# Optimization experiments

Measured on AMD Instinct MI355X. Metric: run time of the kernel, lower is better.

Reference implementation:

```python
import jax, jax.numpy as jnp
import numpy as np

B, L = 128, 100
VOCAB, WORD_D = 50000, 100
TAG_NUM, TAG_D = 52, 20
POS_NUM, POS_D = 202, 20
HID = 256                 # hidden_size = NUM_CAPS * CAP_D
NUM_CAPS, CAP_D = 16, 16
N_CLASS = 19
ROUTING_ITER = 3
IN_D = WORD_D + TAG_D + 2 * POS_D  # 160
ENTITY_MARK = 68          # pos value marking the entity token


def setup_inputs() -> dict:
    key = jax.random.key(0)
    ks = jax.random.split(key, 20)
    s = 0.05
    word = jax.random.randint(ks[0], (B, L), 0, VOCAB)
    tag = jax.random.randint(ks[1], (B, L), 0, TAG_NUM)
    pos1 = jax.random.randint(ks[2], (B, L), 0, POS_NUM)
    pos2 = jax.random.randint(ks[3], (B, L), 0, POS_NUM)
    # guarantee exactly one ENTITY_MARK per row (getEntityFeature's .index(68))
    pos1 = jnp.where(pos1 == ENTITY_MARK, ENTITY_MARK + 1, pos1)
    pos2 = jnp.where(pos2 == ENTITY_MARK, ENTITY_MARK + 1, pos2)
    e1 = jax.random.randint(ks[4], (B,), 0, L)
    e2 = jax.random.randint(ks[5], (B,), 0, L)
    pos1 = pos1.at[jnp.arange(B), e1].set(ENTITY_MARK)
    pos2 = pos2.at[jnp.arange(B), e2].set(ENTITY_MARK)
    # embedding tables (padding_idx 0 rows zeroed for tag/pos, as in torch)
    word_emb = jax.random.normal(ks[6], (VOCAB, WORD_D), jnp.float32) * s
    tag_emb = (jax.random.normal(ks[7], (TAG_NUM, TAG_D), jnp.float32) * s).at[0].set(0.0)
    pos1_emb = (jax.random.normal(ks[8], (POS_NUM, POS_D), jnp.float32) * s).at[0].set(0.0)
    pos2_emb = (jax.random.normal(ks[9], (POS_NUM, POS_D), jnp.float32) * s).at[0].set(0.0)
    # BiLSTM params (torch gate order i,f,g,o stacked along first axis)
    def lstm_params(k):
        k1, k2 = jax.random.split(k)
        w_ih = jax.random.normal(k1, (4 * HID, IN_D), jnp.float32) * s
        w_hh = jax.random.normal(k2, (4 * HID, HID), jnp.float32) * s
        return w_ih, w_hh, jnp.zeros((4 * HID,), jnp.float32), jnp.zeros((4 * HID,), jnp.float32)
    w_ih_f, w_hh_f, b_ih_f, b_hh_f = lstm_params(ks[10])
    w_ih_b, w_hh_b, b_ih_b, b_hh_b = lstm_params(ks[11])
    # digit-caps transform [in_caps, in_dim, out_caps*out_dim]
    W_caps = jax.random.normal(ks[12], (NUM_CAPS * L, CAP_D, N_CLASS * CAP_D), jnp.float32) * s
    b_route = jnp.zeros((NUM_CAPS * L, N_CLASS), jnp.float32)  # routing logit prior (learned)
    return {"word": word, "tag": tag, "pos1": pos1, "pos2": pos2,
            "word_emb": word_emb, "tag_emb": tag_emb, "pos1_emb": pos1_emb, "pos2_emb": pos2_emb,
            "w_ih_f": w_ih_f, "w_hh_f": w_hh_f, "b_ih_f": b_ih_f, "b_hh_f": b_hh_f,
            "w_ih_b": w_ih_b, "w_hh_b": w_hh_b, "b_ih_b": b_ih_b, "b_hh_b": b_hh_b,
            "W_caps": W_caps, "b_route": b_route}


def _lstm_dir(x, w_ih, w_hh, b_ih, b_hh, reverse):
    # x: [B, L, IN_D] -> h: [B, L, HID]
    xg = jnp.einsum('bld,gd->blg', x, w_ih) + b_ih + b_hh  # precompute input gates
    def step(carry, g):
        h, c = carry
        g = g + h @ w_hh.T
        i, f, gg, o = jnp.split(g, 4, axis=-1)
        c = jax.nn.sigmoid(f) * c + jax.nn.sigmoid(i) * jnp.tanh(gg)
        h = jax.nn.sigmoid(o) * jnp.tanh(c)
        return (h, c), h
    init = (jnp.zeros((x.shape[0], HID), x.dtype), jnp.zeros((x.shape[0], HID), x.dtype))
    _, hs = jax.lax.scan(step, init, jnp.swapaxes(xg, 0, 1), reverse=reverse)
    return jnp.swapaxes(hs, 0, 1)


def _squash(x, axis=-1):
    n2 = jnp.sum(x * x, axis=axis, keepdims=True)
    return x * (n2 / (1.0 + n2)) / jnp.sqrt(n2 + 1e-9)


def reference(word, tag, pos1, pos2, word_emb, tag_emb, pos1_emb, pos2_emb,
              w_ih_f, w_hh_f, b_ih_f, b_hh_f, w_ih_b, w_hh_b, b_ih_b, b_hh_b,
              W_caps, b_route):
    # embed + concat (dropout = identity in eval mode)
    emb = jnp.concatenate([word_emb[word], tag_emb[tag], pos1_emb[pos1], pos2_emb[pos2]], axis=-1)
    hf = _lstm_dir(emb, w_ih_f, w_hh_f, b_ih_f, b_hh_f, reverse=False)
    hb = _lstm_dir(emb, w_ih_b, w_hh_b, b_ih_b, b_hh_b, reverse=True)
    x = hf + hb  # sum of direction halves == x[:,:,:H] + x[:,:,H:2H]
    # vectorized entity gather: first index where pos == 68
    bidx = jnp.arange(x.shape[0])
    e1 = jnp.argmax(pos1 == ENTITY_MARK, axis=1)
    e2 = jnp.argmax(pos2 == ENTITY_MARK, axis=1)
    he = x[bidx, e1] + x[bidx, e2]  # [B, HID]
    # primary capsules: [B, L*NUM_CAPS, CAP_D], squashed per capsule
    u = _squash(x.reshape(x.shape[0], L * NUM_CAPS, CAP_D))
    # entity-guided attention over words, broadcast to capsules
    att = jax.nn.softmax(jnp.einsum('bld,bd->bl', x, he), axis=1)  # [B, L]
    alpha = jnp.repeat(att, NUM_CAPS, axis=1)  # [B, L*NUM_CAPS]
    # digit caps predictions: [B, in_caps, N_CLASS, CAP_D]
    u_hat = jnp.einsum('bic,ico->bio', u, W_caps).reshape(x.shape[0], L * NUM_CAPS, N_CLASS, CAP_D)
    # attention-weighted agreement routing
    bb = jnp.broadcast_to(b_route, (x.shape[0],) + b_route.shape)
    v = None
    for _ in range(ROUTING_ITER):
        c = jax.nn.softmax(bb, axis=-1) * alpha[:, :, None]  # coupling * attention
        s = jnp.einsum('bio,biod->bod', c, u_hat)
        v = _squash(s)  # [B, N_CLASS, CAP_D]
        bb = bb + jnp.einsum('biod,bod->bio', u_hat, v)
    # class probabilities = capsule lengths
    return jnp.sqrt(jnp.sum(v * v, axis=2) + 1e-9)
```

## Files before the change

### kernel.cpp

```cpp
#include <hip/hip_runtime.h>
#include <math.h>

#define B_     128
#define L_     100
#define HID_   256
#define IND_   160
#define NCLASS 19
#define CAPD   16
#define NI     1600
#define OD     304
#define ENTITY 68

#define SLDS   24
#define NBT    8
#define BLH    16

typedef _Float16 half2_t __attribute__((ext_vector_type(2)));

__device__ inline half2_t as_h2(unsigned u) {
    union { unsigned u; half2_t h; } x; x.u = u; return x.h;
}
__device__ inline unsigned pack2(float a, float b) {
    union { unsigned u; half2_t h; } x;
    x.h = (half2_t){ (_Float16)a, (_Float16)b };
    return x.u;
}
__device__ inline float fdot2_(unsigned w, unsigned h, float acc) {
#if __has_builtin(__builtin_amdgcn_fdot2)
    return __builtin_amdgcn_fdot2(as_h2(w), as_h2(h), acc, false);
#else
    half2_t wh = as_h2(w), hh = as_h2(h);
    acc = fmaf((float)wh.x, (float)hh.x, acc);
    return fmaf((float)wh.y, (float)hh.y, acc);
#endif
}

__global__ void prep16(const int* __restrict__ word, const int* __restrict__ tag,
                       const int* __restrict__ pos1, const int* __restrict__ pos2,
                       const float* __restrict__ we, const float* __restrict__ te,
                       const float* __restrict__ p1e, const float* __restrict__ p2e,
                       const float* __restrict__ wihf, const float* __restrict__ wihb,
                       const float* __restrict__ whhf, const float* __restrict__ whhb,
                       unsigned* __restrict__ emb16, unsigned* __restrict__ wih16,
                       unsigned* __restrict__ wp16)
{
    int gid = blockIdx.x * 256 + threadIdx.x;
    if (gid < 1024000) {
        int idx = gid;
        int bt = idx / 80;
        int kp = idx - bt * 80;
        int k  = 2 * kp;
        float v0, v1;
        if (k < 100)      { const float* p = we  + word[bt] * 100 + k;         v0 = p[0]; v1 = p[1]; }
        else if (k < 120) { const float* p = te  + tag[bt]  * 20 + (k - 100);  v0 = p[0]; v1 = p[1]; }
        else if (k < 140) { const float* p = p1e + pos1[bt] * 20 + (k - 120);  v0 = p[0]; v1 = p[1]; }
        else              { const float* p = p2e + pos2[bt] * 20 + (k - 140);  v0 = p[0]; v1 = p[1]; }
        emb16[idx] = pack2(v0, v1);
    } else if (gid < 1187840) {
        int idx = gid - 1024000;
        int dir = idx / 81920;
        int rem = idx - dir * 81920;
        int kp  = rem >> 10;
        int gj  = rem & 1023;
        const float* w = dir ? wihb : wihf;
        const float* row = w + (size_t)gj * IND_ + 2 * kp;
        wih16[idx] = pack2(row[0], row[1]);
    } else if (gid < 1449984) {
        int idx = gid - 1187840;
        int g   = idx & 3;
        int h   = (idx >> 2) & 255;
        int p   = (idx >> 10) & 127;
        int dir = idx >> 17;
        const float* whh = dir ? whhb : whhf;
        const float* row = whh + (size_t)(g * 256 + h) * HID_;
        wp16[idx] = pack2(row[2 * p], row[2 * p + 1]);
    }
}

__global__ void __launch_bounds__(256) gemm_xg16(
    const unsigned* __restrict__ emb16, const unsigned* __restrict__ wih16,
    const float* __restrict__ bihf, const float* __restrict__ bhhf,
    const float* __restrict__ bihb, const float* __restrict__ bhhb,
    float* __restrict__ xg)
{
    int gt  = blockIdx.x;
    int t   = blockIdx.y;
    int dir = blockIdx.z;
    const unsigned* wbase = wih16 + (size_t)dir * 81920;
    const float* bi = dir ? bihb : bihf;
    const float* bh = dir ? bhhb : bhhf;
    int gj0 = gt * 128;

    __shared__ unsigned wsh[16][132];
    __shared__ unsigned esh[16][132];

    int tid = threadIdx.x;
    int tx = tid & 15, ty = tid >> 4;

    float acc[8][8];
    #pragma unroll
    for (int i = 0; i < 8; ++i)
        #pragma unroll
        for (int j = 0; j < 8; ++j) acc[i][j] = 0.f;

    for (int kp0 = 0; kp0 < 80; kp0 += 16) {
        __syncthreads();
        #pragma unroll
        for (int m = 0; m < 8; ++m) {
            int e = m * 256 + tid;
            int kw = e >> 7, gw = e & 127;
            wsh[kw][gw] = wbase[(kp0 + kw) * 1024 + gj0 + gw];
            int ke = e & 15, ge = e >> 4;
            esh[ke][ge] = emb16[((size_t)ge * L_ + t) * 80 + kp0 + ke];
        }
        __syncthreads();
        #pragma unroll
        for (int kp = 0; kp < 16; ++kp) {
            unsigned wv[8], ev[8];
            #pragma unroll
            for (int q = 0; q < 8; ++q) wv[q] = wsh[kp][ty * 8 + q];
            #pragma unroll
            for (int q = 0; q < 8; ++q) ev[q] = esh[kp][tx * 8 + q];
            #pragma unroll
            for (int i = 0; i < 8; ++i)
                #pragma unroll
                for (int j = 0; j < 8; ++j) acc[i][j] = fdot2_(wv[i], ev[j], acc[i][j]);
        }
    }
    #pragma unroll
    for (int i = 0; i < 8; ++i) {
        int gj = gj0 + ty * 8 + i;
        float bias = bi[gj] + bh[gj];
        #pragma unroll
        for (int j = 0; j < 8; ++j) {
            int b = tx * 8 + j;
            xg[((((size_t)dir * L_ + t) * 64 + (b >> 1)) * 1024 + gj) * 2 + (b & 1)]
                = acc[i][j] + bias;
        }
    }
}

__global__ void __launch_bounds__(1024, 4) lstm_scan_s(
    const float* __restrict__ xg, const uint4* __restrict__ wp16,
    float* __restrict__ xf2, float* __restrict__ xb2)
{
    int blk = blockIdx.x;
    int dir = blk >> 6;
    int bp  = blk & 63;
    int tid = threadIdx.x;
    int h   = tid & 255;
    int q   = tid >> 8;

    const uint4* wt = wp16 + (size_t)dir * 128 * 256;
    float* xo = dir ? xb2 : xf2;

    __shared__ uint2 hA[128];
    __shared__ uint2 hB[128];
    __shared__ float pbuf[4][8][256];
    __shared__ uint4 wlds[SLDS][256];

    for (int m = q; m < SLDS; m += 4)
        wlds[m][h] = wt[m * 256 + h];

    if (tid < 256) ((unsigned*)hA)[tid] = 0u;
    float c0 = 0.f, c1 = 0.f;
    __syncthreads();

    int pq0  = q * 32;
    int sbeg = (q == 0) ? SLDS : pq0;
    int send = pq0 + 32;

    for (int t = 0; t < L_; ++t) {
        int slot = dir ? (L_ - 1 - t) : t;
        const uint2* hp = (t & 1) ? hB : hA;
        unsigned*    hw = (unsigned*)((t & 1) ? hA : hB);

        float2 gI, gF, gG, gO;
        if (q == 0) {
            const float* xbase = xg + (((size_t)dir * L_ + slot) * 64 + bp) * 2048;
            gI = *(const float2*)(xbase + (0 * 256 + h) * 2);
            gF = *(const float2*)(xbase + (1 * 256 + h) * 2);
            gG = *(const float2*)(xbase + (2 * 256 + h) * 2);
            gO = *(const float2*)(xbase + (3 * 256 + h) * 2);
        }

        float aI0=0.f, aI1=0.f, aF0=0.f, aF1=0.f;
        float aG0=0.f, aG1=0.f, aO0=0.f, aO1=0.f;

        #pragma unroll 8
        for (int p = sbeg; p < send; ++p) {
            uint4 w4 = wt[p * 256 + h];
            uint2 hb = hp[p];
            aI0 = fdot2_(w4.x, hb.x, aI0); aI1 = fdot2_(w4.x, hb.y, aI1);
            aF0 = fdot2_(w4.y, hb.x, aF0); aF1 = fdot2_(w4.y, hb.y, aF1);
            aG0 = fdot2_(w4.z, hb.x, aG0); aG1 = fdot2_(w4.z, hb.y, aG1);
            aO0 = fdot2_(w4.w, hb.x, aO0); aO1 = fdot2_(w4.w, hb.y, aO1);
        }
        if (q == 0) {
            #pragma unroll 8
            for (int p = 0; p < SLDS; ++p) {
                uint4 w4 = wlds[p][h];
                uint2 hb = hp[p];
                aI0 = fdot2_(w4.x, hb.x, aI0); aI1 = fdot2_(w4.x, hb.y, aI1);
                aF0 = fdot2_(w4.y, hb.x, aF0); aF1 = fdot2_(w4.y, hb.y, aF1);
                aG0 = fdot2_(w4.z, hb.x, aG0); aG1 = fdot2_(w4.z, hb.y, aG1);
                aO0 = fdot2_(w4.w, hb.x, aO0); aO1 = fdot2_(w4.w, hb.y, aO1);
            }
        }

        pbuf[q][0][h] = aI0; pbuf[q][1][h] = aI1;
        pbuf[q][2][h] = aF0; pbuf[q][3][h] = aF1;
        pbuf[q][4][h] = aG0; pbuf[q][5][h] = aG1;
        pbuf[q][6][h] = aO0; pbuf[q][7][h] = aO1;
        __syncthreads();

        if (q == 0) {
            float sI0 = pbuf[0][0][h] + pbuf[1][0][h] + pbuf[2][0][h] + pbuf[3][0][h] + gI.x;
            float sI1 = pbuf[0][1][h] + pbuf[1][1][h] + pbuf[2][1][h] + pbuf[3][1][h] + gI.y;
            float sF0 = pbuf[0][2][h] + pbuf[1][2][h] + pbuf[2][2][h] + pbuf[3][2][h] + gF.x;
            float sF1 = pbuf[0][3][h] + pbuf[1][3][h] + pbuf[2][3][h] + pbuf[3][3][h] + gF.y;
            float sG0 = pbuf[0][4][h] + pbuf[1][4][h] + pbuf[2][4][h] + pbuf[3][4][h] + gG.x;
            float sG1 = pbuf[0][5][h] + pbuf[1][5][h] + pbuf[2][5][h] + pbuf[3][5][h] + gG.y;
            float sO0 = pbuf[0][6][h] + pbuf[1][6][h] + pbuf[2][6][h] + pbuf[3][6][h] + gO.x;
            float sO1 = pbuf[0][7][h] + pbuf[1][7][h] + pbuf[2][7][h] + pbuf[3][7][h] + gO.y;

            float i0 = 1.f / (1.f + expf(-sI0));
            float f0 = 1.f / (1.f + expf(-sF0));
            float g0 = tanhf(sG0);
            float o0 = 1.f / (1.f + expf(-sO0));
            c0 = f0 * c0 + i0 * g0;
            float hv0 = o0 * tanhf(c0);

            float i1 = 1.f / (1.f + expf(-sI1));
            float f1 = 1.f / (1.f + expf(-sF1));
            float g1 = tanhf(sG1);
            float o1 = 1.f / (1.f + expf(-sO1));
            c1 = f1 * c1 + i1 * g1;
            float hv1 = o1 * tanhf(c1);

            float n0 = __shfl_xor(hv0, 1);
            float n1 = __shfl_xor(hv1, 1);
            hw[h] = (h & 1) ? pack2(n1, hv1)
                            : pack2(hv0, n0);
            float* xp = xo + ((size_t)slot * 64 + bp) * 512 + h * 2;
            xp[0] = hv0; xp[1] = hv1;
        }
        __syncthreads();
    }
}

__global__ void x_add(const float* __restrict__ xf2, const float* __restrict__ xb2,
                      float* __restrict__ x)
{
    int idx = blockIdx.x * 256 + threadIdx.x;
    int b    = idx & 127;
    int j    = (idx >> 7) & 255;
    int slot = idx >> 15;
    int src  = ((slot * 64 + (b >> 1)) * 512) + j * 2 + (b & 1);
    x[idx] = xf2[src] + xb2[src];
}

__global__ void wc_pack16(const float* __restrict__ W, unsigned* __restrict__ wc)
{
    int gid = blockIdx.x * 256 + threadIdx.x;
    int od  = gid % OD;
    int rest = gid / OD;
    int cp  = rest & 7;
    int i   = rest >> 3;
    float a = W[((size_t)i * 16 + 2 * cp) * OD + od];
    float b = W[((size_t)i * 16 + 2 * cp + 1) * OD + od];
    wc[gid] = pack2(a, b);
}

__global__ void compute_he2(const int* __restrict__ pos1, const int* __restrict__ pos2,
                            const float* __restrict__ x, float* __restrict__ he)
{
    int j = blockIdx.x, b = threadIdx.x;
    int e1 = 0, e2 = 0;
    for (int l = L_ - 1; l >= 0; --l) if (pos1[b * L_ + l] == ENTITY) e1 = l;
    for (int l = L_ - 1; l >= 0; --l) if (pos2[b * L_ + l] == ENTITY) e2 = l;
    he[j * B_ + b] = x[((size_t)e1 * HID_ + j) * B_ + b] + x[((size_t)e2 * HID_ + j) * B_ + b];
}

__global__ void att_logits2(const float* __restrict__ x, const float* __restrict__ he,
                            float* __restrict__ lp)
{
    int l = blockIdx.x, jc = blockIdx.y, b = threadIdx.x;
    int j0 = jc * 32;
    float acc = 0.f;
    #pragma unroll
    for (int jj = 0; jj < 32; ++jj) {
        int j = j0 + jj;
        acc = fmaf(x[((size_t)l * HID_ + j) * B_ + b], he[j * B_ + b], acc);
    }
    lp[((size_t)jc * L_ + l) * B_ + b] = acc;
}

__global__ void att_softmax2(const float* __restrict__ lp, float* __restrict__ att)
{
    int b = blockIdx.x, l = threadIdx.x;
    float val = 0.f;
    if (l < L_) {
        #pragma unroll
        for (int jc = 0; jc < 8; ++jc) val += lp[((size_t)jc * L_ + l) * B_ + b];
    }
    __shared__ float red[128];
    red[l] = (l < L_) ? val : -1e30f;
    __syncthreads();
    for (int off = 64; off > 0; off >>= 1) {
        if (l < off) red[l] = fmaxf(red[l], red[l + off]);
        __syncthreads();
    }
    float m = red[0];
    __syncthreads();
    float e = (l < L_) ? expf(val - m) : 0.f;
    red[l] = e;
    __syncthreads();
    for (int off = 64; off > 0; off >>= 1) {
        if (l < off) red[l] += red[l + off];
        __syncthreads();
    }
    float inv = 1.f / red[0];
    if (l < L_) att[l * B_ + b] = e * inv;
}

__global__ void u_squash16(const float* __restrict__ x, unsigned* __restrict__ u16)
{
    int i = blockIdx.x, b = threadIdx.x;
    int l = i >> 4, cap = i & 15;
    float vals[16]; float n2 = 0.f;
    #pragma unroll
    for (int c2 = 0; c2 < 16; ++c2) {
        float v = x[((size_t)l * HID_ + cap * 16 + c2) * B_ + b];
        vals[c2] = v; n2 = fmaf(v, v, n2);
    }
    float f = (n2 / (1.f + n2)) / sqrtf(n2 + 1e-9f);
    #pragma unroll
    for (int cp = 0; cp < 8; ++cp)
        u16[((size_t)i * B_ + b) * 8 + cp] = pack2(vals[2 * cp] * f, vals[2 * cp + 1] * f);
}

__global__ void __launch_bounds__(320) s_pass16(
    const unsigned* __restrict__ u16, const unsigned* __restrict__ Wc16,
    const float* __restrict__ bb, const float* __restrict__ br, int first,
    const float* __restrict__ att, float* __restrict__ partial)
{
    int ic = blockIdx.x, bt = blockIdx.y;
    int i0 = ic * 16, b0 = bt * BLH;
    __shared__ float C[BLH][16][20];
    int tid = threadIdx.x;
    for (int e = tid; e < BLH * 16; e += 320) {
        int bl = e >> 4, il = e & 15;
        int b = b0 + bl, i = i0 + il;
        const float* bbp = first ? (br + (size_t)i * NCLASS)
                                 : (bb + ((size_t)b * NI + i) * NCLASS);
        float m = bbp[0];
        #pragma unroll
        for (int o = 1; o < NCLASS; ++o) m = fmaxf(m, bbp[o]);
        float s = 0.f; float e2[NCLASS];
        #pragma unroll
        for (int o = 0; o < NCLASS; ++o) { e2[o] = expf(bbp[o] - m); s += e2[o]; }
        float al = att[(i >> 4) * B_ + b] / s;
        #pragma unroll
        for (int o = 0; o < NCLASS; ++o) C[bl][il][o] = e2[o] * al;
    }
    __syncthreads();
    if (tid >= OD) return;
    int od = tid, o = od >> 4;
    float acc[BLH];
    #pragma unroll
    for (int bl = 0; bl < BLH; ++bl) acc[bl] = 0.f;
    for (int il = 0; il < 16; ++il) {
        int i = i0 + il;
        const unsigned* wp = Wc16 + (size_t)i * 8 * OD + od;
        unsigned w2[8];
        #pragma unroll
        for (int cp = 0; cp < 8; ++cp) w2[cp] = wp[cp * OD];
        const unsigned* up = u16 + ((size_t)i * B_ + b0) * 8;
        #pragma unroll
        for (int bl = 0; bl < BLH; ++bl) {
            float uh = 0.f;
            #pragma unroll
            for (int cp = 0; cp < 8; ++cp) uh = fdot2_(up[bl * 8 + cp], w2[cp], uh);
            acc[bl] = fmaf(C[bl][il][o], uh, acc[bl]);
        }
    }
    #pragma unroll
    for (int bl = 0; bl < BLH; ++bl)
        partial[((size_t)ic * B_ + b0 + bl) * OD + od] = acc[bl];
}

__global__ void __launch_bounds__(320) sreduce_squash(
    const float* __restrict__ partial, float* __restrict__ v,
    float* __restrict__ out, int write_out)
{
    int b = blockIdx.x;
    int od = threadIdx.x;
    if (od >= OD) return;
    float acc = 0.f;
    for (int ic = 0; ic < 100; ++ic) acc += partial[((size_t)ic * B_ + b) * OD + od];
    float n2 = acc * acc;
    n2 += __shfl_xor(n2, 1); n2 += __shfl_xor(n2, 2);
    n2 += __shfl_xor(n2, 4); n2 += __shfl_xor(n2, 8);
    float f = (n2 / (1.f + n2)) / sqrtf(n2 + 1e-9f);
    float vv = acc * f;
    v[(size_t)b * OD + od] = vv;
    if (write_out) {
        float n2v = vv * vv;
        n2v += __shfl_xor(n2v, 1); n2v += __shfl_xor(n2v, 2);
        n2v += __shfl_xor(n2v, 4); n2v += __shfl_xor(n2v, 8);
        if ((od & 15) == 0) out[b * NCLASS + (od >> 4)] = sqrtf(n2v + 1e-9f);
    }
}

__global__ void __launch_bounds__(320) bb_pass16(
    const unsigned* __restrict__ u16, const unsigned* __restrict__ Wc16,
    const float* __restrict__ v, float* __restrict__ bb,
    const float* __restrict__ br, int first)
{
    int ic = blockIdx.x, bt = blockIdx.y;
    int i0 = ic * 16, b0 = bt * BLH;
    int tid = threadIdx.x;
    if (tid >= OD) return;
    int od = tid, o = od >> 4, d = od & 15;
    float vv[BLH];
    #pragma unroll
    for (int bl = 0; bl < BLH; ++bl) vv[bl] = v[(size_t)(b0 + bl) * OD + od];
    for (int il = 0; il < 16; ++il) {
        int i = i0 + il;
        const unsigned* wp = Wc16 + (size_t)i * 8 * OD + od;
        unsigned w2[8];
        #pragma unroll
        for (int cp = 0; cp < 8; ++cp) w2[cp] = wp[cp * OD];
        const unsigned* up = u16 + ((size_t)i * B_ + b0) * 8;
        #pragma unroll
        for (int bl = 0; bl < BLH; ++bl) {
            float uh = 0.f;
            #pragma unroll
            for (int cp = 0; cp < 8; ++cp) uh = fdot2_(up[bl * 8 + cp], w2[cp], uh);
            float p = uh * vv[bl];
            p += __shfl_xor(p, 1);
            p += __shfl_xor(p, 2);
            p += __shfl_xor(p, 4);
            p += __shfl_xor(p, 8);
            if (d == 0) {
                size_t off = ((size_t)(b0 + bl) * NI + i) * NCLASS + o;
                bb[off] = (first ? br[(size_t)i * NCLASS + o] : bb[off]) + p;
            }
        }
    }
}

extern "C" void kernel_launch(void* const* d_in, const int* in_sizes, int n_in,
                              void* d_out, int out_size, void* d_ws, size_t ws_size,
                              hipStream_t stream)
{
    (void)in_sizes; (void)n_in; (void)out_size; (void)ws_size;
    const int*   word = (const int*)d_in[0];
    const int*   tag  = (const int*)d_in[1];
    const int*   pos1 = (const int*)d_in[2];
    const int*   pos2 = (const int*)d_in[3];
    const float* we   = (const float*)d_in[4];
    const float* te   = (const float*)d_in[5];
    const float* p1e  = (const float*)d_in[6];
    const float* p2e  = (const float*)d_in[7];
    const float* wihf = (const float*)d_in[8];
    const float* whhf = (const float*)d_in[9];
    const float* bihf = (const float*)d_in[10];
    const float* bhhf = (const float*)d_in[11];
    const float* wihb = (const float*)d_in[12];
    const float* whhb = (const float*)d_in[13];
    const float* bihb = (const float*)d_in[14];
    const float* bhhb = (const float*)d_in[15];
    const float* Wc   = (const float*)d_in[16];
    const float* br   = (const float*)d_in[17];

    float* wsp = (float*)d_ws;
    unsigned* emb16 = (unsigned*)wsp;
    unsigned* wih16 = (unsigned*)(wsp + 1024000);
    unsigned* wp16  = (unsigned*)(wsp + 1024000 + 163840);
    float* xg  = wsp + 2048000;
    float* xf  = xg + 26214400;
    float* xb  = xf + 3276800;
    float* he  = xb + 3276800;
    float* att = he + 32768;
    unsigned* Wc16 = (unsigned*)xf;
    float*    lp   = xf + 3891200;
    float*    x    = xg;
    unsigned* u16  = (unsigned*)(xg + 3276800);
    float*    bb   = xg + 6553600;
    float*    part = xg + 10444800;
    float*    s    = xg + 14336000;
    float*    v    = s + 38912;
    float*    out  = (float*)d_out;

    prep16<<<5665, 256, 0, stream>>>(word, tag, pos1, pos2, we, te, p1e, p2e,
                                     wihf, wihb, whhf, whhb, emb16, wih16, wp16);
    gemm_xg16<<<dim3(8, 100, 2), 256, 0, stream>>>(emb16, wih16, bihf, bhhf, bihb, bhhb, xg);
    lstm_scan_s<<<128, 1024, 0, stream>>>(xg, (const uint4*)wp16, xf, xb);
    x_add<<<12800, 256, 0, stream>>>(xf, xb, x);
    wc_pack16<<<15200, 256, 0, stream>>>(Wc, Wc16);
    compute_he2<<<256, 128, 0, stream>>>(pos1, pos2, x, he);
    att_logits2<<<dim3(100, 8), 128, 0, stream>>>(x, he, lp);
    att_softmax2<<<128, 128, 0, stream>>>(lp, att);
    u_squash16<<<1600, 128, 0, stream>>>(x, u16);
    for (int it = 0; it < 3; ++it) {
        s_pass16<<<dim3(100, NBT), 320, 0, stream>>>(u16, Wc16, bb, br, it == 0, att, part);
        sreduce_squash<<<128, 320, 0, stream>>>(part, v, out, (it == 2) ? 1 : 0);
        if (it < 2) bb_pass16<<<dim3(100, NBT), 320, 0, stream>>>(u16, Wc16, v, bb, br, it == 0);
    }
}
```

Before: 1.078 ms.

## Stream LSTM recurrent weights as FP8 and decode to fp16 in scan

Adds an FP8 (e4m3) packed copy of the recurrent weight matrix, built in the prep kernel. The scan loop's global-memory weight reads use it, halving bytes per step, and each pair is converted to fp16 before the dot2 accumulation. The LDS-resident slice still uses fp16. This cuts memory traffic in the latency-bound recurrence but reduces weight precision and adds per-element conversion instructions.

```diff
diff --git a/kernel.cpp b/kernel.cpp
--- a/kernel.cpp
+++ b/kernel.cpp
@@ -25,7 +25,7 @@
     x.h = (half2_t){ (_Float16)a, (_Float16)b };
     return x.u;
 }
-__device__ inline float fdot2_(unsigned w, unsigned h, float acc) {
+__device__ inline float dot2f(unsigned w, unsigned h, float acc) {
 #if __has_builtin(__builtin_amdgcn_fdot2)
     return __builtin_amdgcn_fdot2(as_h2(w), as_h2(h), acc, false);
 #else
@@ -35,6 +35,59 @@
 #endif
 }
 
+__device__ inline unsigned sw_e4m3(float x) {
+    float ax = fabsf(x);
+    unsigned s = (x < 0.f) ? 0x80u : 0u;
+    if (ax >= 448.f) return s | 0x7e;
+    if (ax < 0.015625f) {
+        int q = (int)rintf(ax * 512.0f);
+        if (q >= 8) return s | 0x08;
+        return s | (unsigned)q;
+    }
+    union { float f; unsigned u; } c; c.f = ax;
+    int e32 = (int)((c.u >> 23) & 0xff) - 127;
+    unsigned man = c.u & 0x7fffff;
+    unsigned m3 = man >> 20;
+    unsigned rem = man & 0xfffff;
+    if (rem > 0x80000 || (rem == 0x80000 && (m3 & 1))) {
+        m3 += 1;
+        if (m3 == 8) { m3 = 0; e32 += 1; if (e32 > 8) return s | 0x7e; }
+    }
+    return s | ((unsigned)(e32 + 7) << 3) | m3;
+}
+template <bool HI>
+__device__ inline unsigned pack_fp8x2(float a, float b, unsigned old) {
+#if __has_builtin(__builtin_amdgcn_cvt_pk_fp8_f32)
+    return (unsigned)__builtin_amdgcn_cvt_pk_fp8_f32(a, b, (int)old, HI);
+#else
+    unsigned w = sw_e4m3(a) | (sw_e4m3(b) << 8);
+    return HI ? ((old & 0x0000ffffu) | (w << 16)) : ((old & 0xffff0000u) | w);
+#endif
+}
+__device__ inline unsigned dec_e4m3_f16(unsigned v) {
+    unsigned s = (v & 0x80) << 8;
+    unsigned e = (v >> 3) & 0xf;
+    unsigned m = v & 7;
+    if (e == 0) {
+        if (m == 0) return s;
+        int sh = (m & 4) ? 0 : ((m & 2) ? 1 : 2);
+        unsigned e16 = (unsigned)(15 - 9 + (2 - sh));
+        unsigned man = (m << (sh + 1)) & 0x7;
+        return s | (e16 << 10) | (man << 7);
+    }
+    return s | ((e + 8) << 10) | (m << 7);
+}
+template <bool HI>
+__device__ inline unsigned fp8pair_to_h2(unsigned src) {
+#if __has_builtin(__builtin_amdgcn_cvt_pk_f32_fp8)
+    auto f = __builtin_amdgcn_cvt_pk_f32_fp8((int)src, HI);
+    return pack2(f[0], f[1]);
+#else
+    unsigned w = HI ? (src >> 16) : (src & 0xffffu);
+    return dec_e4m3_f16(w & 0xff) | (dec_e4m3_f16((w >> 8) & 0xff) << 16);
+#endif
+}
+
 __global__ void prep16(const int* __restrict__ word, const int* __restrict__ tag,
                        const int* __restrict__ pos1, const int* __restrict__ pos2,
                        const float* __restrict__ we, const float* __restrict__ te,
@@ -42,7 +95,7 @@
                        const float* __restrict__ wihf, const float* __restrict__ wihb,
                        const float* __restrict__ whhf, const float* __restrict__ whhb,
                        unsigned* __restrict__ emb16, unsigned* __restrict__ wih16,
-                       unsigned* __restrict__ wp16)
+                       unsigned* __restrict__ wp16, uint2* __restrict__ wp8)
 {
     int gid = blockIdx.x * 256 + threadIdx.x;
     if (gid < 1024000) {
@@ -74,6 +127,22 @@
         const float* whh = dir ? whhb : whhf;
         const float* row = whh + (size_t)(g * 256 + h) * HID_;
         wp16[idx] = pack2(row[2 * p], row[2 * p + 1]);
+    } else if (gid < 1515520) {
+        int idx = gid - 1449984;
+        int h   = idx & 255;
+        int p   = (idx >> 8) & 127;
+        int dir = idx >> 15;
+        const float* whh = dir ? whhb : whhf;
+        unsigned lo = 0, hi = 0;
+        lo = pack_fp8x2<false>(whh[(size_t)(0 * 256 + h) * HID_ + 2 * p],
+                               whh[(size_t)(0 * 256 + h) * HID_ + 2 * p + 1], lo);
+        lo = pack_fp8x2<true>(whh[(size_t)(1 * 256 + h) * HID_ + 2 * p],
+                              whh[(size_t)(1 * 256 + h) * HID_ + 2 * p + 1], lo);
+        hi = pack_fp8x2<false>(whh[(size_t)(2 * 256 + h) * HID_ + 2 * p],
+                               whh[(size_t)(2 * 256 + h) * HID_ + 2 * p + 1], hi);
+        hi = pack_fp8x2<true>(whh[(size_t)(3 * 256 + h) * HID_ + 2 * p],
+                              whh[(size_t)(3 * 256 + h) * HID_ + 2 * p + 1], hi);
+        wp8[idx] = make_uint2(lo, hi);
     }
 }
 
@@ -124,7 +193,8 @@
             #pragma unroll
             for (int i = 0; i < 8; ++i)
                 #pragma unroll
-                for (int j = 0; j < 8; ++j) acc[i][j] = fdot2_(wv[i], ev[j], acc[i][j]);
+                for (int j = 0; j < 8; ++j)
+                    acc[i][j] = dot2f(wv[i], ev[j], acc[i][j]);
         }
     }
     #pragma unroll
@@ -140,9 +210,9 @@
     }
 }
 
-__global__ void __launch_bounds__(1024, 4) lstm_scan_s(
+__global__ void __launch_bounds__(1024, 4) lstm_scan_8(
     const float* __restrict__ xg, const uint4* __restrict__ wp16,
-    float* __restrict__ xf2, float* __restrict__ xb2)
+    const uint2* __restrict__ wp8, float* __restrict__ xf2, float* __restrict__ xb2)
 {
     int blk = blockIdx.x;
     int dir = blk >> 6;
@@ -151,7 +221,8 @@
     int h   = tid & 255;
     int q   = tid >> 8;
 
-    const uint4* wt = wp16 + (size_t)dir * 128 * 256;
+    const uint4* wt  = wp16 + (size_t)dir * 128 * 256;
+    const uint2* wt8 = wp8  + ((size_t)dir << 15);
     float* xo = dir ? xb2 : xf2;
 
     __shared__ uint2 hA[128];
@@ -189,22 +260,26 @@
 
         #pragma unroll 8
         for (int p = sbeg; p < send; ++p) {
-            uint4 w4 = wt[p * 256 + h];
+            uint2 w8 = wt8[p * 256 + h];
             uint2 hb = hp[p];
-            aI0 = fdot2_(w4.x, hb.x, aI0); aI1 = fdot2_(w4.x, hb.y, aI1);
-            aF0 = fdot2_(w4.y, hb.x, aF0); aF1 = fdot2_(w4.y, hb.y, aF1);
-            aG0 = fdot2_(w4.z, hb.x, aG0); aG1 = fdot2_(w4.z, hb.y, aG1);
-            aO0 = fdot2_(w4.w, hb.x, aO0); aO1 = fdot2_(w4.w, hb.y, aO1);
+            unsigned wI = fp8pair_to_h2<false>(w8.x);
+            unsigned wF = fp8pair_to_h2<true>(w8.x);
+            unsigned wG = fp8pair_to_h2<false>(w8.y);
+            unsigned wO = fp8pair_to_h2<true>(w8.y);
+            aI0 = dot2f(wI, hb.x, aI0); aI1 = dot2f(wI, hb.y, aI1);
+            aF0 = dot2f(wF, hb.x, aF0); aF1 = dot2f(wF, hb.y, aF1);
+            aG0 = dot2f(wG, hb.x, aG0); aG1 = dot2f(wG, hb.y, aG1);
+            aO0 = dot2f(wO, hb.x, aO0); aO1 = dot2f(wO, hb.y, aO1);
         }
         if (q == 0) {
             #pragma unroll 8
             for (int p = 0; p < SLDS; ++p) {
                 uint4 w4 = wlds[p][h];
                 uint2 hb = hp[p];
-                aI0 = fdot2_(w4.x, hb.x, aI0); aI1 = fdot2_(w4.x, hb.y, aI1);
-                aF0 = fdot2_(w4.y, hb.x, aF0); aF1 = fdot2_(w4.y, hb.y, aF1);
-                aG0 = fdot2_(w4.z, hb.x, aG0); aG1 = fdot2_(w4.z, hb.y, aG1);
-                aO0 = fdot2_(w4.w, hb.x, aO0); aO1 = fdot2_(w4.w, hb.y, aO1);
+                aI0 = dot2f(w4.x, hb.x, aI0); aI1 = dot2f(w4.x, hb.y, aI1);
+                aF0 = dot2f(w4.y, hb.x, aF0); aF1 = dot2f(w4.y, hb.y, aF1);
+                aG0 = dot2f(w4.z, hb.x, aG0); aG1 = dot2f(w4.z, hb.y, aG1);
+                aO0 = dot2f(w4.w, hb.x, aO0); aO1 = dot2f(w4.w, hb.y, aO1);
             }
         }
 
@@ -381,7 +456,7 @@
         for (int bl = 0; bl < BLH; ++bl) {
             float uh = 0.f;
             #pragma unroll
-            for (int cp = 0; cp < 8; ++cp) uh = fdot2_(up[bl * 8 + cp], w2[cp], uh);
+            for (int cp = 0; cp < 8; ++cp) uh = dot2f(up[bl * 8 + cp], w2[cp], uh);
             acc[bl] = fmaf(C[bl][il][o], uh, acc[bl]);
         }
     }
@@ -437,7 +512,7 @@
         for (int bl = 0; bl < BLH; ++bl) {
             float uh = 0.f;
             #pragma unroll
-            for (int cp = 0; cp < 8; ++cp) uh = fdot2_(up[bl * 8 + cp], w2[cp], uh);
+            for (int cp = 0; cp < 8; ++cp) uh = dot2f(up[bl * 8 + cp], w2[cp], uh);
             float p = uh * vv[bl];
             p += __shfl_xor(p, 1);
             p += __shfl_xor(p, 2);
@@ -479,6 +554,7 @@
     unsigned* emb16 = (unsigned*)wsp;
     unsigned* wih16 = (unsigned*)(wsp + 1024000);
     unsigned* wp16  = (unsigned*)(wsp + 1024000 + 163840);
+    uint2*    wp8   = (uint2*)(wsp + 1449984);
     float* xg  = wsp + 2048000;
     float* xf  = xg + 26214400;
     float* xb  = xf + 3276800;
@@ -494,10 +570,10 @@
     float*    v    = s + 38912;
     float*    out  = (float*)d_out;
 
-    prep16<<<5665, 256, 0, stream>>>(word, tag, pos1, pos2, we, te, p1e, p2e,
-                                     wihf, wihb, whhf, whhb, emb16, wih16, wp16);
+    prep16<<<5920, 256, 0, stream>>>(word, tag, pos1, pos2, we, te, p1e, p2e,
+                                     wihf, wihb, whhf, whhb, emb16, wih16, wp16, wp8);
     gemm_xg16<<<dim3(8, 100, 2), 256, 0, stream>>>(emb16, wih16, bihf, bhhf, bihb, bhhb, xg);
-    lstm_scan_s<<<128, 1024, 0, stream>>>(xg, (const uint4*)wp16, xf, xb);
+    lstm_scan_8<<<128, 1024, 0, stream>>>(xg, (const uint4*)wp16, wp8, xf, xb);
     x_add<<<12800, 256, 0, stream>>>(xf, xb, x);
     wc_pack16<<<15200, 256, 0, stream>>>(Wc, Wc16);
     compute_he2<<<256, 128, 0, stream>>>(pos1, pos2, x, he);
```

Result: slower. 1.281 ms (+18.9%).
